# Optimization experiments

Measured on AMD Instinct MI355X. Metric: run time of the kernel, lower is better.

The kernel has to match this reference:

```python
import jax, jax.numpy as jnp
import numpy as np

DIM = 128
HEADS = 4
LOGIT_MAX = float(np.log(1.0 / 0.01))  # log(100)


def setup_inputs() -> dict:
    root = jax.random.key(0)
    ks = jax.random.split(root, 10)
    B, nH, nW, Lq, Lv, C = 16, 16, 16, 64, 64, DIM
    s = 0.02
    return {
        "query": jax.random.normal(ks[0], (B, nH, nW, Lq, C), jnp.float32),
        "key": jax.random.normal(ks[1], (B, nH, nW, Lv, C), jnp.float32),
        "value": jax.random.normal(ks[2], (B, nH, nW, Lv, C), jnp.float32),
        "position": jax.random.normal(ks[3], (B, HEADS, Lq, Lv), jnp.float32),
        # torch nn.Linear convention: weight [out_features, in_features]
        "Wq": jax.random.normal(ks[4], (C, C), jnp.float32) * s,
        "bq": jnp.zeros((C,), jnp.float32),
        "Wk": jax.random.normal(ks[5], (C, C), jnp.float32) * s,  # fc_key has no bias
        "Wv": jax.random.normal(ks[6], (C, C), jnp.float32) * s,
        "bv": jnp.zeros((C,), jnp.float32),
        "Wp": jax.random.normal(ks[7], (C, C), jnp.float32) * s,
        "bp": jnp.zeros((C,), jnp.float32),
        "logit_scale": jnp.log(10.0) * jnp.ones((HEADS, 1, 1), jnp.float32),
    }


def reference(query, key, value, position, Wq, bq, Wk, Wv, bv, Wp, bp, logit_scale):
    B, nH, nW, Lq, C = query.shape
    Lv = key.shape[3]
    H = logit_scale.shape[0]
    d = C // H
    # QKV projections, split heads: [B,nH,nW,H,L,d]
    q = (query @ Wq.T + bq).reshape(B, nH, nW, Lq, H, d).swapaxes(3, 4)
    k = (key @ Wk.T).reshape(B, nH, nW, Lv, H, d).swapaxes(3, 4)
    v = (value @ Wv.T + bv).reshape(B, nH, nW, Lv, H, d).swapaxes(3, 4)
    # clamped learned per-head logit scale
    scale = jnp.exp(jnp.minimum(logit_scale, LOGIT_MAX))  # [H,1,1]
    attn = jnp.einsum('bijhqd,bijhkd->bijhqk', q, k) * scale
    attn = attn + position[:, None, None]  # broadcast over window grid (nH,nW)
    attn = jax.nn.softmax(attn, axis=-1)
    x = jnp.einsum('bijhqk,bijhkd->bijhqd', attn, v)
    x = x.swapaxes(3, 4).reshape(B, nH, nW, Lq, C)
    x = x @ Wp.T + bp
    return (x, attn)
```

## Files before the change

### kernel.cpp

```cpp
#include <hip/hip_runtime.h>

using f16   = _Float16;
using f16x4 = __attribute__((ext_vector_type(4))) _Float16;
using f16x8 = __attribute__((ext_vector_type(8))) _Float16;
using f32x4 = __attribute__((ext_vector_type(4))) float;

#define DEVI __device__ __forceinline__

namespace {
constexpr int S_XQ  = 0;
constexpr int S_XK  = 16384;
constexpr int S_SCR = 32768;
constexpr float LOGIT_MAX_C = 4.6051701859880914f;
constexpr float L2E = 1.4426950408889634f;
}

DEVI int swzA(int row, int b) { return (row << 8) + (b ^ ((row & 7) << 4)); }
DEVI int swz64(int row, int b) { return (row << 6) + (b ^ (((row >> 1) & 3) << 4)); }

DEVI f16x8 ldA(const char* base, int row, int k0) {
  return *reinterpret_cast<const f16x8*>(base + swzA(row, k0 << 1));
}

DEVI void stage_in(const float* __restrict__ src, char* __restrict__ dst, int tid) {
#pragma unroll
  for (int i = 0; i < 8; ++i) {
    int f = tid + (i << 8);
    float4 v = reinterpret_cast<const float4*>(src)[f];
    f16x4 h;
    h[0] = (f16)v.x; h[1] = (f16)v.y; h[2] = (f16)v.z; h[3] = (f16)v.w;
    *reinterpret_cast<f16x4*>(dst + swzA(f >> 5, (f & 31) << 3)) = h;
  }
}

DEVI void proj_acc(const char* __restrict__ xb, const f16* __restrict__ Wm,
                   f32x4 (&acc)[4][2], int w, int lr, int lg) {
#pragma unroll
  for (int mt = 0; mt < 4; ++mt)
#pragma unroll
    for (int n = 0; n < 2; ++n)
      acc[mt][n] = f32x4{0.f, 0.f, 0.f, 0.f};
#pragma unroll
  for (int kt = 0; kt < 4; ++kt) {
    f16x8 b0 = *reinterpret_cast<const f16x8*>(Wm + (w * 32 + lr) * 128 + kt * 32 + lg * 8);
    f16x8 b1 = *reinterpret_cast<const f16x8*>(Wm + (w * 32 + 16 + lr) * 128 + kt * 32 + lg * 8);
#pragma unroll
    for (int mt = 0; mt < 4; ++mt) {
      f16x8 a = ldA(xb, mt * 16 + lr, kt * 32 + lg * 8);
      acc[mt][0] = __builtin_amdgcn_mfma_f32_16x16x32_f16(a, b0, acc[mt][0], 0, 0, 0);
      acc[mt][1] = __builtin_amdgcn_mfma_f32_16x16x32_f16(a, b1, acc[mt][1], 0, 0, 0);
    }
  }
}

DEVI void epi_scr64(const f32x4 (&acc)[4][2], char* __restrict__ scr,
                    const float* __restrict__ bias, int lr, int lg) {
  float b0 = bias ? bias[lr] : 0.f;
  float b1 = bias ? bias[16 + lr] : 0.f;
#pragma unroll
  for (int mt = 0; mt < 4; ++mt)
#pragma unroll
    for (int n = 0; n < 2; ++n)
#pragma unroll
      for (int r = 0; r < 4; ++r) {
        int row = mt * 16 + lg * 4 + r;
        *reinterpret_cast<f16*>(scr + swz64(row, (n * 16 + lr) << 1)) =
            (f16)(acc[mt][n][r] + (n ? b1 : b0));
      }
}
DEVI f16x8 ldS64(const char* __restrict__ scr, int row, int lg) {
  return *reinterpret_cast<const f16x8*>(scr + swz64(row, lg << 4));
}

DEVI void epi_rowmajor(const f32x4 (&acc)[4][2], char* __restrict__ dst,
                       int w, int lr, int lg) {
#pragma unroll
  for (int mt = 0; mt < 4; ++mt)
#pragma unroll
    for (int n = 0; n < 2; ++n)
#pragma unroll
      for (int r = 0; r < 4; ++r) {
        int row = mt * 16 + lg * 4 + r;
        int col = w * 32 + n * 16 + lr;
        *reinterpret_cast<f16*>(dst + swzA(row, col << 1)) = (f16)acc[mt][n][r];
      }
}

__global__ void wcvt_kernel(const float* __restrict__ Wq, const float* __restrict__ Wk,
                            const float* __restrict__ Wv, const float* __restrict__ Wp,
                            f16* __restrict__ W16) {
  int idx = blockIdx.x * 256 + threadIdx.x;
  int m = idx >> 12;
  int off = (idx & 4095) << 2;
  const float* src = m == 0 ? Wq : m == 1 ? Wk : m == 2 ? Wv : Wp;
  float4 v = *reinterpret_cast<const float4*>(src + off);
  f16x4 h;
  h[0] = (f16)v.x; h[1] = (f16)v.y; h[2] = (f16)v.z; h[3] = (f16)v.w;
  *reinterpret_cast<f16x4*>(W16 + (m << 14) + off) = h;
}

__global__ __launch_bounds__(256, 3)
void fpca_kernel(const float* __restrict__ q_in, const float* __restrict__ k_in,
                 const float* __restrict__ v_in, const float* __restrict__ pos_in,
                 const f16* __restrict__ W16,
                 const float* __restrict__ bq, const float* __restrict__ bv,
                 const float* __restrict__ bp, const float* __restrict__ lsc,
                 float* __restrict__ d_x, float* __restrict__ d_attn) {
  __shared__ char smem[49152];
  const int tid = threadIdx.x;
  const int w = tid >> 6;
  const int lane = tid & 63;
  const int lr = lane & 15;
  const int lg = lane >> 4;
  const int win = blockIdx.x;
  const int b = win >> 8;
  const size_t winOff = (size_t)win << 13;
  const f16* Wq16 = W16;
  const f16* Wk16 = W16 + 16384;
  const f16* Wv16 = W16 + 32768;
  const f16* Wp16 = W16 + 49152;
  char* scr = smem + S_SCR + (w << 12);

  stage_in(q_in + winOff, smem + S_XQ, tid);
  stage_in(k_in + winOff, smem + S_XK, tid);
  const float4* vsrc = reinterpret_cast<const float4*>(v_in + winOff);
  f16x4 pfh[8];
#pragma unroll
  for (int i = 0; i < 8; ++i) {
    float4 v = vsrc[tid + (i << 8)];
    pfh[i][0] = (f16)v.x; pfh[i][1] = (f16)v.y;
    pfh[i][2] = (f16)v.z; pfh[i][3] = (f16)v.w;
  }
  __syncthreads();

  f32x4 acc[4][2];
  proj_acc(smem + S_XQ, Wq16, acc, w, lr, lg);
  epi_scr64(acc, scr, bq + w * 32, lr, lg);
  f16x8 bQ[4];
#pragma unroll
  for (int nt = 0; nt < 4; ++nt) bQ[nt] = ldS64(scr, nt * 16 + lr, lg);

  proj_acc(smem + S_XK, Wk16, acc, w, lr, lg);
  epi_scr64(acc, scr, nullptr, lr, lg);
  f16x8 aK[4];
#pragma unroll
  for (int mt = 0; mt < 4; ++mt) aK[mt] = ldS64(scr, mt * 16 + lr, lg);
  __syncthreads();

#pragma unroll
  for (int i = 0; i < 8; ++i) {
    int f = tid + (i << 8);
    *reinterpret_cast<f16x4*>(smem + S_XK + swzA(f >> 5, (f & 31) << 3)) = pfh[i];
  }

  const float scale = exp2f(fminf(lsc[w], LOGIT_MAX_C) * L2E);
  const float* pos = pos_in + (((size_t)b * 4 + w) << 12);
  float* attn_out = d_attn + (((size_t)win * 4 + w) << 12);
  f16x4 P16[4][4];
#pragma unroll
  for (int nt = 0; nt < 4; ++nt) {
    f32x4 s[4];
#pragma unroll
    for (int mt = 0; mt < 4; ++mt) s[mt] = f32x4{0.f, 0.f, 0.f, 0.f};
#pragma unroll
    for (int mt = 0; mt < 4; ++mt)
      s[mt] = __builtin_amdgcn_mfma_f32_16x16x32_f16(aK[mt], bQ[nt], s[mt], 0, 0, 0);
    const int q = nt * 16 + lr;
#pragma unroll
    for (int mt = 0; mt < 4; ++mt) {
      float4 pv = *reinterpret_cast<const float4*>(pos + (q << 6) + mt * 16 + lg * 4);
      s[mt][0] = s[mt][0] * scale + pv.x;
      s[mt][1] = s[mt][1] * scale + pv.y;
      s[mt][2] = s[mt][2] * scale + pv.z;
      s[mt][3] = s[mt][3] * scale + pv.w;
    }
    float m = s[0][0];
#pragma unroll
    for (int mt = 0; mt < 4; ++mt)
#pragma unroll
      for (int r = 0; r < 4; ++r) m = fmaxf(m, s[mt][r]);
    m = fmaxf(m, __shfl_xor(m, 16));
    m = fmaxf(m, __shfl_xor(m, 32));
    float sum = 0.f;
#pragma unroll
    for (int mt = 0; mt < 4; ++mt)
#pragma unroll
      for (int r = 0; r < 4; ++r) {
        float e = exp2f((s[mt][r] - m) * L2E);
        s[mt][r] = e;
        sum += e;
      }
    sum += __shfl_xor(sum, 16);
    sum += __shfl_xor(sum, 32);
    float rinv = __builtin_amdgcn_rcpf(sum);
#pragma unroll
    for (int mt = 0; mt < 4; ++mt) {
      float4 o;
      o.x = (s[mt][0] *= rinv);
      o.y = (s[mt][1] *= rinv);
      o.z = (s[mt][2] *= rinv);
      o.w = (s[mt][3] *= rinv);
      *reinterpret_cast<float4*>(attn_out + (q << 6) + mt * 16 + lg * 4) = o;
      P16[mt][nt][0] = (f16)s[mt][0];
      P16[mt][nt][1] = (f16)s[mt][1];
      P16[mt][nt][2] = (f16)s[mt][2];
      P16[mt][nt][3] = (f16)s[mt][3];
    }
  }

#define WR_P(MT)                                                                   \
  {                                                                                \
    _Pragma("unroll") for (int nt = 0; nt < 4; ++nt) {                             \
      const int q = nt * 16 + lr;                                                  \
      *reinterpret_cast<f16x4*>(scr + (q << 6) +                                   \
          (((((MT) & 1) << 5) + (lg << 3)) ^ (((q >> 1) & 3) << 4))) =             \
          P16[MT][nt];                                                             \
    }                                                                              \
  }
  f16x8 aP[4][2];
#pragma unroll
  for (int h = 0; h < 2; ++h) {
    WR_P(2 * h)
    WR_P(2 * h + 1)
#pragma unroll
    for (int mt = 0; mt < 4; ++mt) {
      const int q = mt * 16 + lr;
      aP[mt][h] = *reinterpret_cast<const f16x8*>(scr + (q << 6) +
          ((lg << 4) ^ (((q >> 1) & 3) << 4)));
    }
  }
  __syncthreads();

  proj_acc(smem + S_XK, Wv16, acc, w, lr, lg);
  {
    float c0 = bv[w * 32 + lr], c1 = bv[w * 32 + 16 + lr];
#pragma unroll
    for (int mt = 0; mt < 4; ++mt)
#pragma unroll
      for (int n = 0; n < 2; ++n) {
        int d = n * 16 + lr;
        f16x4 h;
        h[0] = (f16)(acc[mt][n][0] + (n ? c1 : c0));
        h[1] = (f16)(acc[mt][n][1] + (n ? c1 : c0));
        h[2] = (f16)(acc[mt][n][2] + (n ? c1 : c0));
        h[3] = (f16)(acc[mt][n][3] + (n ? c1 : c0));
        *reinterpret_cast<f16x4*>(scr + (d << 7) +
            ((mt * 32 + lg * 8) ^ ((d & 7) << 4))) = h;
      }
  }
  f16x8 bV[2][2];
#pragma unroll
  for (int n = 0; n < 2; ++n)
#pragma unroll
    for (int kt = 0; kt < 2; ++kt) {
      int d = n * 16 + lr;
      bV[n][kt] = *reinterpret_cast<const f16x8*>(scr + (d << 7) +
          ((kt * 64 + lg * 16) ^ ((d & 7) << 4)));
    }

  f32x4 oacc[4][2];
#pragma unroll
  for (int mt = 0; mt < 4; ++mt)
#pragma unroll
    for (int n = 0; n < 2; ++n)
      oacc[mt][n] = f32x4{0.f, 0.f, 0.f, 0.f};
#pragma unroll
  for (int mt = 0; mt < 4; ++mt)
#pragma unroll
    for (int kt = 0; kt < 2; ++kt) {
      oacc[mt][0] = __builtin_amdgcn_mfma_f32_16x16x32_f16(aP[mt][kt], bV[0][kt], oacc[mt][0], 0, 0, 0);
      oacc[mt][1] = __builtin_amdgcn_mfma_f32_16x16x32_f16(aP[mt][kt], bV[1][kt], oacc[mt][1], 0, 0, 0);
    }

  epi_rowmajor(oacc, smem + S_XQ, w, lr, lg);
  __syncthreads();

  f32x4 xacc[4][2];
  proj_acc(smem + S_XQ, Wp16, xacc, w, lr, lg);
  const float b0 = bp[w * 32 + lr];
  const float b1 = bp[w * 32 + 16 + lr];
  float* xo = d_x + winOff;
#pragma unroll
  for (int mt = 0; mt < 4; ++mt)
#pragma unroll
    for (int n = 0; n < 2; ++n)
#pragma unroll
      for (int r = 0; r < 4; ++r) {
        int row = mt * 16 + lg * 4 + r;
        int col = w * 32 + n * 16 + lr;
        xo[(row << 7) + col] = xacc[mt][n][r] + (n ? b1 : b0);
      }
}

extern "C" void kernel_launch(void* const* d_in, const int* in_sizes, int n_in,
                              void* d_out, int out_size, void* d_ws, size_t ws_size,
                              hipStream_t stream) {
  const float* q   = (const float*)d_in[0];
  const float* k   = (const float*)d_in[1];
  const float* v   = (const float*)d_in[2];
  const float* pos = (const float*)d_in[3];
  const float* Wq  = (const float*)d_in[4];
  const float* bq  = (const float*)d_in[5];
  const float* Wk  = (const float*)d_in[6];
  const float* Wv  = (const float*)d_in[7];
  const float* bv  = (const float*)d_in[8];
  const float* Wp  = (const float*)d_in[9];
  const float* bp  = (const float*)d_in[10];
  const float* ls  = (const float*)d_in[11];
  f16* W16 = (f16*)d_ws;
  float* d_x    = (float*)d_out;
  float* d_attn = d_x + (size_t)16 * 16 * 16 * 64 * 128;
  wcvt_kernel<<<64, 256, 0, stream>>>(Wq, Wk, Wv, Wp, W16);
  fpca_kernel<<<4096, 256, 0, stream>>>(q, k, v, pos, W16, bq, bv, bp, ls,
                                        d_x, d_attn);
}
```

Baseline: 205.6 us.

## Load value operand directly from global and drop two block barriers

The value projection now reads fp32 value rows straight from global memory into MFMA A-operands, converting them on the fly. This replaces the register prefetch, the LDS staging and the barrier that guarded it. The attention output is written to each wave's own scratch slice, and the output projection reads across those four slices, which removes the row-major epilogue and the barrier before the V projection. Fewer barriers and no LDS round trip for V, at the cost of uncoalesced 32-byte global reads per lane that are repeated across the four waves, and the loss of the early V prefetch overlap.

New measurement: 273.4 us. +33.0%, slower.

```diff
diff --git a/kernel.cpp b/kernel.cpp
--- a/kernel.cpp
+++ b/kernel.cpp
@@ -33,6 +33,15 @@
   }
 }
 
+DEVI f16x8 ld_g8(const float* __restrict__ G, int row, int k0) {
+  const float4* p = reinterpret_cast<const float4*>(G + row * 128 + k0);
+  float4 a = p[0], c = p[1];
+  f16x8 r;
+  r[0] = (f16)a.x; r[1] = (f16)a.y; r[2] = (f16)a.z; r[3] = (f16)a.w;
+  r[4] = (f16)c.x; r[5] = (f16)c.y; r[6] = (f16)c.z; r[7] = (f16)c.w;
+  return r;
+}
+
 DEVI void proj_acc(const char* __restrict__ xb, const f16* __restrict__ Wm,
                    f32x4 (&acc)[4][2], int w, int lr, int lg) {
 #pragma unroll
@@ -70,20 +79,6 @@
 }
 DEVI f16x8 ldS64(const char* __restrict__ scr, int row, int lg) {
   return *reinterpret_cast<const f16x8*>(scr + swz64(row, lg << 4));
-}
-
-DEVI void epi_rowmajor(const f32x4 (&acc)[4][2], char* __restrict__ dst,
-                       int w, int lr, int lg) {
-#pragma unroll
-  for (int mt = 0; mt < 4; ++mt)
-#pragma unroll
-    for (int n = 0; n < 2; ++n)
-#pragma unroll
-      for (int r = 0; r < 4; ++r) {
-        int row = mt * 16 + lg * 4 + r;
-        int col = w * 32 + n * 16 + lr;
-        *reinterpret_cast<f16*>(dst + swzA(row, col << 1)) = (f16)acc[mt][n][r];
-      }
 }
 
 __global__ void wcvt_kernel(const float* __restrict__ Wq, const float* __restrict__ Wk,
@@ -123,14 +118,6 @@
 
   stage_in(q_in + winOff, smem + S_XQ, tid);
   stage_in(k_in + winOff, smem + S_XK, tid);
-  const float4* vsrc = reinterpret_cast<const float4*>(v_in + winOff);
-  f16x4 pfh[8];
-#pragma unroll
-  for (int i = 0; i < 8; ++i) {
-    float4 v = vsrc[tid + (i << 8)];
-    pfh[i][0] = (f16)v.x; pfh[i][1] = (f16)v.y;
-    pfh[i][2] = (f16)v.z; pfh[i][3] = (f16)v.w;
-  }
   __syncthreads();
 
   f32x4 acc[4][2];
@@ -145,13 +132,6 @@
   f16x8 aK[4];
 #pragma unroll
   for (int mt = 0; mt < 4; ++mt) aK[mt] = ldS64(scr, mt * 16 + lr, lg);
-  __syncthreads();
-
-#pragma unroll
-  for (int i = 0; i < 8; ++i) {
-    int f = tid + (i << 8);
-    *reinterpret_cast<f16x4*>(smem + S_XK + swzA(f >> 5, (f & 31) << 3)) = pfh[i];
-  }
 
   const float scale = exp2f(fminf(lsc[w], LOGIT_MAX_C) * L2E);
   const float* pos = pos_in + (((size_t)b * 4 + w) << 12);
@@ -229,9 +209,27 @@
           ((lg << 4) ^ (((q >> 1) & 3) << 4)));
     }
   }
-  __syncthreads();
-
-  proj_acc(smem + S_XK, Wv16, acc, w, lr, lg);
+#undef WR_P
+
+  {
+    const float* Xv = v_in + winOff;
+#pragma unroll
+    for (int mt = 0; mt < 4; ++mt)
+#pragma unroll
+      for (int n = 0; n < 2; ++n)
+        acc[mt][n] = f32x4{0.f, 0.f, 0.f, 0.f};
+#pragma unroll
+    for (int kt = 0; kt < 4; ++kt) {
+      f16x8 b0 = *reinterpret_cast<const f16x8*>(Wv16 + (w * 32 + lr) * 128 + kt * 32 + lg * 8);
+      f16x8 b1 = *reinterpret_cast<const f16x8*>(Wv16 + (w * 32 + 16 + lr) * 128 + kt * 32 + lg * 8);
+#pragma unroll
+      for (int mt = 0; mt < 4; ++mt) {
+        f16x8 a = ld_g8(Xv, mt * 16 + lr, kt * 32 + lg * 8);
+        acc[mt][0] = __builtin_amdgcn_mfma_f32_16x16x32_f16(a, b0, acc[mt][0], 0, 0, 0);
+        acc[mt][1] = __builtin_amdgcn_mfma_f32_16x16x32_f16(a, b1, acc[mt][1], 0, 0, 0);
+      }
+    }
+  }
   {
     float c0 = bv[w * 32 + lr], c1 = bv[w * 32 + 16 + lr];
 #pragma unroll
@@ -272,11 +270,27 @@
       oacc[mt][1] = __builtin_amdgcn_mfma_f32_16x16x32_f16(aP[mt][kt], bV[1][kt], oacc[mt][1], 0, 0, 0);
     }
 
-  epi_rowmajor(oacc, smem + S_XQ, w, lr, lg);
+  epi_scr64(oacc, scr, nullptr, lr, lg);
   __syncthreads();
 
   f32x4 xacc[4][2];
-  proj_acc(smem + S_XQ, Wp16, xacc, w, lr, lg);
+#pragma unroll
+  for (int mt = 0; mt < 4; ++mt)
+#pragma unroll
+    for (int n = 0; n < 2; ++n)
+      xacc[mt][n] = f32x4{0.f, 0.f, 0.f, 0.f};
+#pragma unroll
+  for (int kt = 0; kt < 4; ++kt) {
+    const char* oscr = smem + S_SCR + (kt << 12);
+    f16x8 b0 = *reinterpret_cast<const f16x8*>(Wp16 + (w * 32 + lr) * 128 + kt * 32 + lg * 8);
+    f16x8 b1 = *reinterpret_cast<const f16x8*>(Wp16 + (w * 32 + 16 + lr) * 128 + kt * 32 + lg * 8);
+#pragma unroll
+    for (int mt = 0; mt < 4; ++mt) {
+      f16x8 a = ldS64(oscr, mt * 16 + lr, lg);
+      xacc[mt][0] = __builtin_amdgcn_mfma_f32_16x16x32_f16(a, b0, xacc[mt][0], 0, 0, 0);
+      xacc[mt][1] = __builtin_amdgcn_mfma_f32_16x16x32_f16(a, b1, xacc[mt][1], 0, 0, 0);
+    }
+  }
   const float b0 = bp[w * 32 + lr];
   const float b1 = bp[w * 32 + 16 + lr];
   float* xo = d_x + winOff;
```

## Replace LDS scratch transposes with cross-lane shuffles for Q/K/V/P fragments

Applied to the files above, without the earlier changes.

Q and K projections are now computed transposed (weights as the A operand), so the accumulator layout can be rearranged into MFMA operand fragments with lane shuffles instead of a round trip through per-wave LDS scratch. The V and P fragment handoffs also move from LDS stores and loads to shuffle-based gathers. This removes the 16 KB scratch region, cutting shared memory per block from 48 KB to 32 KB, which could allow more resident blocks. The cost is many ds_bpermute-style shuffles and selects per fragment, and possibly higher register pressure.

Result: slower. 238.0 us (+15.8%).

```diff
diff --git a/kernel.cpp b/kernel.cpp
--- a/kernel.cpp
+++ b/kernel.cpp
@@ -8,15 +8,13 @@
 #define DEVI __device__ __forceinline__
 
 namespace {
-constexpr int S_XQ  = 0;
-constexpr int S_XK  = 16384;
-constexpr int S_SCR = 32768;
+constexpr int S_XQ = 0;
+constexpr int S_XK = 16384;
 constexpr float LOGIT_MAX_C = 4.6051701859880914f;
 constexpr float L2E = 1.4426950408889634f;
 }
 
 DEVI int swzA(int row, int b) { return (row << 8) + (b ^ ((row & 7) << 4)); }
-DEVI int swz64(int row, int b) { return (row << 6) + (b ^ (((row >> 1) & 3) << 4)); }
 
 DEVI f16x8 ldA(const char* base, int row, int k0) {
   return *reinterpret_cast<const f16x8*>(base + swzA(row, k0 << 1));
@@ -33,6 +31,55 @@
   }
 }
 
+DEVI f16x4 shfl4(f16x4 v, int src) {
+  int2 t = __builtin_bit_cast(int2, v);
+  int2 r;
+  r.x = __shfl(t.x, src);
+  r.y = __shfl(t.y, src);
+  return __builtin_bit_cast(f16x4, r);
+}
+DEVI f16x8 gather_frag(f16x4 p0, f16x4 p1, int s0, int s1, int lg) {
+  f16x4 a0 = shfl4(p0, s0), a1 = shfl4(p0, s1);
+  f16x4 b0 = shfl4(p1, s0), b1 = shfl4(p1, s1);
+  f16x4 lo = (lg & 2) ? b0 : a0;
+  f16x4 hi = (lg & 2) ? b1 : a1;
+  f16x8 r;
+  r[0] = lo[0]; r[1] = lo[1]; r[2] = lo[2]; r[3] = lo[3];
+  r[4] = hi[0]; r[5] = hi[1]; r[6] = hi[2]; r[7] = hi[3];
+  return r;
+}
+DEVI f16x4 pack4(f32x4 a) {
+  f16x4 h;
+  h[0] = (f16)a[0]; h[1] = (f16)a[1]; h[2] = (f16)a[2]; h[3] = (f16)a[3];
+  return h;
+}
+DEVI f16x4 pack4b(f32x4 a, float4 b) {
+  f16x4 h;
+  h[0] = (f16)(a[0] + b.x); h[1] = (f16)(a[1] + b.y);
+  h[2] = (f16)(a[2] + b.z); h[3] = (f16)(a[3] + b.w);
+  return h;
+}
+
+DEVI void projT_acc(const char* __restrict__ xb, const f16* __restrict__ Wm,
+                    f32x4 (&acc)[2][4], int w, int lr, int lg) {
+#pragma unroll
+  for (int ft = 0; ft < 2; ++ft)
+#pragma unroll
+    for (int t = 0; t < 4; ++t)
+      acc[ft][t] = f32x4{0.f, 0.f, 0.f, 0.f};
+#pragma unroll
+  for (int kt = 0; kt < 4; ++kt) {
+    f16x8 w0 = *reinterpret_cast<const f16x8*>(Wm + (w * 32 + lr) * 128 + kt * 32 + lg * 8);
+    f16x8 w1 = *reinterpret_cast<const f16x8*>(Wm + (w * 32 + 16 + lr) * 128 + kt * 32 + lg * 8);
+#pragma unroll
+    for (int t = 0; t < 4; ++t) {
+      f16x8 x = ldA(xb, t * 16 + lr, kt * 32 + lg * 8);
+      acc[0][t] = __builtin_amdgcn_mfma_f32_16x16x32_f16(w0, x, acc[0][t], 0, 0, 0);
+      acc[1][t] = __builtin_amdgcn_mfma_f32_16x16x32_f16(w1, x, acc[1][t], 0, 0, 0);
+    }
+  }
+}
+
 DEVI void proj_acc(const char* __restrict__ xb, const f16* __restrict__ Wm,
                    f32x4 (&acc)[4][2], int w, int lr, int lg) {
 #pragma unroll
@@ -51,25 +98,6 @@
       acc[mt][1] = __builtin_amdgcn_mfma_f32_16x16x32_f16(a, b1, acc[mt][1], 0, 0, 0);
     }
   }
-}
-
-DEVI void epi_scr64(const f32x4 (&acc)[4][2], char* __restrict__ scr,
-                    const float* __restrict__ bias, int lr, int lg) {
-  float b0 = bias ? bias[lr] : 0.f;
-  float b1 = bias ? bias[16 + lr] : 0.f;
-#pragma unroll
-  for (int mt = 0; mt < 4; ++mt)
-#pragma unroll
-    for (int n = 0; n < 2; ++n)
-#pragma unroll
-      for (int r = 0; r < 4; ++r) {
-        int row = mt * 16 + lg * 4 + r;
-        *reinterpret_cast<f16*>(scr + swz64(row, (n * 16 + lr) << 1)) =
-            (f16)(acc[mt][n][r] + (n ? b1 : b0));
-      }
-}
-DEVI f16x8 ldS64(const char* __restrict__ scr, int row, int lg) {
-  return *reinterpret_cast<const f16x8*>(scr + swz64(row, lg << 4));
 }
 
 DEVI void epi_rowmajor(const f32x4 (&acc)[4][2], char* __restrict__ dst,
@@ -106,12 +134,14 @@
                  const float* __restrict__ bq, const float* __restrict__ bv,
                  const float* __restrict__ bp, const float* __restrict__ lsc,
                  float* __restrict__ d_x, float* __restrict__ d_attn) {
-  __shared__ char smem[49152];
+  __shared__ char smem[32768];
   const int tid = threadIdx.x;
   const int w = tid >> 6;
   const int lane = tid & 63;
   const int lr = lane & 15;
   const int lg = lane >> 4;
+  const int s0 = lr + ((lane & 16) << 1);
+  const int s1 = s0 + 16;
   const int win = blockIdx.x;
   const int b = win >> 8;
   const size_t winOff = (size_t)win << 13;
@@ -119,7 +149,6 @@
   const f16* Wk16 = W16 + 16384;
   const f16* Wv16 = W16 + 32768;
   const f16* Wp16 = W16 + 49152;
-  char* scr = smem + S_SCR + (w << 12);
 
   stage_in(q_in + winOff, smem + S_XQ, tid);
   stage_in(k_in + winOff, smem + S_XK, tid);
@@ -133,18 +162,20 @@
   }
   __syncthreads();
 
-  f32x4 acc[4][2];
-  proj_acc(smem + S_XQ, Wq16, acc, w, lr, lg);
-  epi_scr64(acc, scr, bq + w * 32, lr, lg);
+  f32x4 accT[2][4];
+  projT_acc(smem + S_XQ, Wq16, accT, w, lr, lg);
+  float4 bq0 = *reinterpret_cast<const float4*>(bq + w * 32 + lg * 4);
+  float4 bq1 = *reinterpret_cast<const float4*>(bq + w * 32 + 16 + lg * 4);
   f16x8 bQ[4];
 #pragma unroll
-  for (int nt = 0; nt < 4; ++nt) bQ[nt] = ldS64(scr, nt * 16 + lr, lg);
-
-  proj_acc(smem + S_XK, Wk16, acc, w, lr, lg);
-  epi_scr64(acc, scr, nullptr, lr, lg);
+  for (int nt = 0; nt < 4; ++nt)
+    bQ[nt] = gather_frag(pack4b(accT[0][nt], bq0), pack4b(accT[1][nt], bq1), s0, s1, lg);
+
+  projT_acc(smem + S_XK, Wk16, accT, w, lr, lg);
   f16x8 aK[4];
 #pragma unroll
-  for (int mt = 0; mt < 4; ++mt) aK[mt] = ldS64(scr, mt * 16 + lr, lg);
+  for (int mt = 0; mt < 4; ++mt)
+    aK[mt] = gather_frag(pack4(accT[0][mt]), pack4(accT[1][mt]), s0, s1, lg);
   __syncthreads();
 
 #pragma unroll
@@ -207,56 +238,27 @@
       P16[mt][nt][3] = (f16)s[mt][3];
     }
   }
-
-#define WR_P(MT)                                                                   \
-  {                                                                                \
-    _Pragma("unroll") for (int nt = 0; nt < 4; ++nt) {                             \
-      const int q = nt * 16 + lr;                                                  \
-      *reinterpret_cast<f16x4*>(scr + (q << 6) +                                   \
-          (((((MT) & 1) << 5) + (lg << 3)) ^ (((q >> 1) & 3) << 4))) =             \
-          P16[MT][nt];                                                             \
-    }                                                                              \
-  }
-  f16x8 aP[4][2];
-#pragma unroll
-  for (int h = 0; h < 2; ++h) {
-    WR_P(2 * h)
-    WR_P(2 * h + 1)
-#pragma unroll
-    for (int mt = 0; mt < 4; ++mt) {
-      const int q = mt * 16 + lr;
-      aP[mt][h] = *reinterpret_cast<const f16x8*>(scr + (q << 6) +
-          ((lg << 4) ^ (((q >> 1) & 3) << 4)));
-    }
-  }
   __syncthreads();
 
-  proj_acc(smem + S_XK, Wv16, acc, w, lr, lg);
+  f32x4 vacc[4][2];
+  proj_acc(smem + S_XK, Wv16, vacc, w, lr, lg);
+  f16x8 bV[2][2];
   {
     float c0 = bv[w * 32 + lr], c1 = bv[w * 32 + 16 + lr];
 #pragma unroll
-    for (int mt = 0; mt < 4; ++mt)
-#pragma unroll
-      for (int n = 0; n < 2; ++n) {
-        int d = n * 16 + lr;
-        f16x4 h;
-        h[0] = (f16)(acc[mt][n][0] + (n ? c1 : c0));
-        h[1] = (f16)(acc[mt][n][1] + (n ? c1 : c0));
-        h[2] = (f16)(acc[mt][n][2] + (n ? c1 : c0));
-        h[3] = (f16)(acc[mt][n][3] + (n ? c1 : c0));
-        *reinterpret_cast<f16x4*>(scr + (d << 7) +
-            ((mt * 32 + lg * 8) ^ ((d & 7) << 4))) = h;
+    for (int n = 0; n < 2; ++n) {
+      float c = n ? c1 : c0;
+      f16x4 pV[4];
+#pragma unroll
+      for (int mt = 0; mt < 4; ++mt) {
+        f32x4 t = vacc[mt][n];
+        t[0] += c; t[1] += c; t[2] += c; t[3] += c;
+        pV[mt] = pack4(t);
       }
-  }
-  f16x8 bV[2][2];
-#pragma unroll
-  for (int n = 0; n < 2; ++n)
-#pragma unroll
-    for (int kt = 0; kt < 2; ++kt) {
-      int d = n * 16 + lr;
-      bV[n][kt] = *reinterpret_cast<const f16x8*>(scr + (d << 7) +
-          ((kt * 64 + lg * 16) ^ ((d & 7) << 4)));
-    }
+      bV[n][0] = gather_frag(pV[0], pV[1], s0, s1, lg);
+      bV[n][1] = gather_frag(pV[2], pV[3], s0, s1, lg);
+    }
+  }
 
   f32x4 oacc[4][2];
 #pragma unroll
@@ -265,11 +267,12 @@
     for (int n = 0; n < 2; ++n)
       oacc[mt][n] = f32x4{0.f, 0.f, 0.f, 0.f};
 #pragma unroll
-  for (int mt = 0; mt < 4; ++mt)
-#pragma unroll
-    for (int kt = 0; kt < 2; ++kt) {
-      oacc[mt][0] = __builtin_amdgcn_mfma_f32_16x16x32_f16(aP[mt][kt], bV[0][kt], oacc[mt][0], 0, 0, 0);
-      oacc[mt][1] = __builtin_amdgcn_mfma_f32_16x16x32_f16(aP[mt][kt], bV[1][kt], oacc[mt][1], 0, 0, 0);
+  for (int kt = 0; kt < 2; ++kt)
+#pragma unroll
+    for (int mt = 0; mt < 4; ++mt) {
+      f16x8 aPx = gather_frag(P16[2 * kt][mt], P16[2 * kt + 1][mt], s0, s1, lg);
+      oacc[mt][0] = __builtin_amdgcn_mfma_f32_16x16x32_f16(aPx, bV[0][kt], oacc[mt][0], 0, 0, 0);
+      oacc[mt][1] = __builtin_amdgcn_mfma_f32_16x16x32_f16(aPx, bV[1][kt], oacc[mt][1], 0, 0, 0);
     }
 
   epi_rowmajor(oacc, smem + S_XQ, w, lr, lg);
```

## Split each window across 8 warps by halving query rows per warp

Applied to the files above, without the earlier changes.

The block grows from 256 to 512 threads, so each head is handled by two warps that each own half of the 64 query/token rows. Projections, softmax, PV and the output projection are all split by row half. Shared-memory scratch is reorganised into per-head Q/K regions plus per-warp P scratch, and extra barriers are added so K and V can be shared across the two halves. The aim is more waves per window and lower per-thread register pressure to hide latency. The cost is more LDS (64KB per block), extra synchronisation, and duplicated weight-fragment loads per warp.

Result: slower. 253.3 us (+23.2%).

```diff
diff --git a/kernel.cpp b/kernel.cpp
--- a/kernel.cpp
+++ b/kernel.cpp
@@ -24,8 +24,8 @@
 
 DEVI void stage_in(const float* __restrict__ src, char* __restrict__ dst, int tid) {
 #pragma unroll
-  for (int i = 0; i < 8; ++i) {
-    int f = tid + (i << 8);
+  for (int i = 0; i < 4; ++i) {
+    int f = tid + (i << 9);
     float4 v = reinterpret_cast<const float4*>(src)[f];
     f16x4 h;
     h[0] = (f16)v.x; h[1] = (f16)v.y; h[2] = (f16)v.z; h[3] = (f16)v.w;
@@ -33,57 +33,43 @@
   }
 }
 
-DEVI void proj_acc(const char* __restrict__ xb, const f16* __restrict__ Wm,
-                   f32x4 (&acc)[4][2], int w, int lr, int lg) {
-#pragma unroll
-  for (int mt = 0; mt < 4; ++mt)
-#pragma unroll
-    for (int n = 0; n < 2; ++n)
-      acc[mt][n] = f32x4{0.f, 0.f, 0.f, 0.f};
+DEVI void proj_split(const char* __restrict__ xb, const f16* __restrict__ Wm,
+                     f32x4 (&acc)[2][2], int w, int hf, int lr, int lg) {
+#pragma unroll
+  for (int mtl = 0; mtl < 2; ++mtl)
+#pragma unroll
+    for (int n = 0; n < 2; ++n)
+      acc[mtl][n] = f32x4{0.f, 0.f, 0.f, 0.f};
 #pragma unroll
   for (int kt = 0; kt < 4; ++kt) {
     f16x8 b0 = *reinterpret_cast<const f16x8*>(Wm + (w * 32 + lr) * 128 + kt * 32 + lg * 8);
     f16x8 b1 = *reinterpret_cast<const f16x8*>(Wm + (w * 32 + 16 + lr) * 128 + kt * 32 + lg * 8);
 #pragma unroll
-    for (int mt = 0; mt < 4; ++mt) {
-      f16x8 a = ldA(xb, mt * 16 + lr, kt * 32 + lg * 8);
-      acc[mt][0] = __builtin_amdgcn_mfma_f32_16x16x32_f16(a, b0, acc[mt][0], 0, 0, 0);
-      acc[mt][1] = __builtin_amdgcn_mfma_f32_16x16x32_f16(a, b1, acc[mt][1], 0, 0, 0);
-    }
-  }
-}
-
-DEVI void epi_scr64(const f32x4 (&acc)[4][2], char* __restrict__ scr,
-                    const float* __restrict__ bias, int lr, int lg) {
+    for (int mtl = 0; mtl < 2; ++mtl) {
+      f16x8 a = ldA(xb, hf * 32 + mtl * 16 + lr, kt * 32 + lg * 8);
+      acc[mtl][0] = __builtin_amdgcn_mfma_f32_16x16x32_f16(a, b0, acc[mtl][0], 0, 0, 0);
+      acc[mtl][1] = __builtin_amdgcn_mfma_f32_16x16x32_f16(a, b1, acc[mtl][1], 0, 0, 0);
+    }
+  }
+}
+
+DEVI void epi_half(const f32x4 (&acc)[2][2], char* __restrict__ scr,
+                   const float* __restrict__ bias, int hf, int lr, int lg) {
   float b0 = bias ? bias[lr] : 0.f;
   float b1 = bias ? bias[16 + lr] : 0.f;
 #pragma unroll
-  for (int mt = 0; mt < 4; ++mt)
+  for (int mtl = 0; mtl < 2; ++mtl)
 #pragma unroll
     for (int n = 0; n < 2; ++n)
 #pragma unroll
       for (int r = 0; r < 4; ++r) {
-        int row = mt * 16 + lg * 4 + r;
+        int row = hf * 32 + mtl * 16 + lg * 4 + r;
         *reinterpret_cast<f16*>(scr + swz64(row, (n * 16 + lr) << 1)) =
-            (f16)(acc[mt][n][r] + (n ? b1 : b0));
+            (f16)(acc[mtl][n][r] + (n ? b1 : b0));
       }
 }
 DEVI f16x8 ldS64(const char* __restrict__ scr, int row, int lg) {
   return *reinterpret_cast<const f16x8*>(scr + swz64(row, lg << 4));
-}
-
-DEVI void epi_rowmajor(const f32x4 (&acc)[4][2], char* __restrict__ dst,
-                       int w, int lr, int lg) {
-#pragma unroll
-  for (int mt = 0; mt < 4; ++mt)
-#pragma unroll
-    for (int n = 0; n < 2; ++n)
-#pragma unroll
-      for (int r = 0; r < 4; ++r) {
-        int row = mt * 16 + lg * 4 + r;
-        int col = w * 32 + n * 16 + lr;
-        *reinterpret_cast<f16*>(dst + swzA(row, col << 1)) = (f16)acc[mt][n][r];
-      }
 }
 
 __global__ void wcvt_kernel(const float* __restrict__ Wq, const float* __restrict__ Wk,
@@ -99,16 +85,18 @@
   *reinterpret_cast<f16x4*>(W16 + (m << 14) + off) = h;
 }
 
-__global__ __launch_bounds__(256, 3)
+__global__ __launch_bounds__(512, 4)
 void fpca_kernel(const float* __restrict__ q_in, const float* __restrict__ k_in,
                  const float* __restrict__ v_in, const float* __restrict__ pos_in,
                  const f16* __restrict__ W16,
                  const float* __restrict__ bq, const float* __restrict__ bv,
                  const float* __restrict__ bp, const float* __restrict__ lsc,
                  float* __restrict__ d_x, float* __restrict__ d_attn) {
-  __shared__ char smem[49152];
+  __shared__ char smem[65536];
   const int tid = threadIdx.x;
-  const int w = tid >> 6;
+  const int W = tid >> 6;
+  const int w = W & 3;
+  const int hf = W >> 2;
   const int lane = tid & 63;
   const int lr = lane & 15;
   const int lg = lane >> 4;
@@ -119,53 +107,56 @@
   const f16* Wk16 = W16 + 16384;
   const f16* Wv16 = W16 + 32768;
   const f16* Wp16 = W16 + 49152;
-  char* scr = smem + S_SCR + (w << 12);
+  char* Qscr = smem + S_SCR + (w << 13);
+  char* Kscr = Qscr + 4096;
+  char* Pscr = smem + S_XQ + (W << 11);
 
   stage_in(q_in + winOff, smem + S_XQ, tid);
   stage_in(k_in + winOff, smem + S_XK, tid);
   const float4* vsrc = reinterpret_cast<const float4*>(v_in + winOff);
-  f16x4 pfh[8];
-#pragma unroll
-  for (int i = 0; i < 8; ++i) {
-    float4 v = vsrc[tid + (i << 8)];
+  f16x4 pfh[4];
+#pragma unroll
+  for (int i = 0; i < 4; ++i) {
+    float4 v = vsrc[tid + (i << 9)];
     pfh[i][0] = (f16)v.x; pfh[i][1] = (f16)v.y;
     pfh[i][2] = (f16)v.z; pfh[i][3] = (f16)v.w;
   }
   __syncthreads();
 
-  f32x4 acc[4][2];
-  proj_acc(smem + S_XQ, Wq16, acc, w, lr, lg);
-  epi_scr64(acc, scr, bq + w * 32, lr, lg);
-  f16x8 bQ[4];
-#pragma unroll
-  for (int nt = 0; nt < 4; ++nt) bQ[nt] = ldS64(scr, nt * 16 + lr, lg);
-
-  proj_acc(smem + S_XK, Wk16, acc, w, lr, lg);
-  epi_scr64(acc, scr, nullptr, lr, lg);
+  f32x4 acc[2][2];
+  proj_split(smem + S_XQ, Wq16, acc, w, hf, lr, lg);
+  epi_half(acc, Qscr, bq + w * 32, hf, lr, lg);
+  f16x8 bQ[2];
+#pragma unroll
+  for (int ntl = 0; ntl < 2; ++ntl)
+    bQ[ntl] = ldS64(Qscr, hf * 32 + ntl * 16 + lr, lg);
+
+  proj_split(smem + S_XK, Wk16, acc, w, hf, lr, lg);
+  epi_half(acc, Kscr, nullptr, hf, lr, lg);
+  __syncthreads();
+
+#pragma unroll
+  for (int i = 0; i < 4; ++i) {
+    int f = tid + (i << 9);
+    *reinterpret_cast<f16x4*>(smem + S_XK + swzA(f >> 5, (f & 31) << 3)) = pfh[i];
+  }
   f16x8 aK[4];
 #pragma unroll
-  for (int mt = 0; mt < 4; ++mt) aK[mt] = ldS64(scr, mt * 16 + lr, lg);
-  __syncthreads();
-
-#pragma unroll
-  for (int i = 0; i < 8; ++i) {
-    int f = tid + (i << 8);
-    *reinterpret_cast<f16x4*>(smem + S_XK + swzA(f >> 5, (f & 31) << 3)) = pfh[i];
-  }
+  for (int mt = 0; mt < 4; ++mt) aK[mt] = ldS64(Kscr, mt * 16 + lr, lg);
 
   const float scale = exp2f(fminf(lsc[w], LOGIT_MAX_C) * L2E);
   const float* pos = pos_in + (((size_t)b * 4 + w) << 12);
   float* attn_out = d_attn + (((size_t)win * 4 + w) << 12);
-  f16x4 P16[4][4];
-#pragma unroll
-  for (int nt = 0; nt < 4; ++nt) {
+  f16x4 P16[4][2];
+#pragma unroll
+  for (int ntl = 0; ntl < 2; ++ntl) {
     f32x4 s[4];
 #pragma unroll
     for (int mt = 0; mt < 4; ++mt) s[mt] = f32x4{0.f, 0.f, 0.f, 0.f};
 #pragma unroll
     for (int mt = 0; mt < 4; ++mt)
-      s[mt] = __builtin_amdgcn_mfma_f32_16x16x32_f16(aK[mt], bQ[nt], s[mt], 0, 0, 0);
-    const int q = nt * 16 + lr;
+      s[mt] = __builtin_amdgcn_mfma_f32_16x16x32_f16(aK[mt], bQ[ntl], s[mt], 0, 0, 0);
+    const int q = hf * 32 + ntl * 16 + lr;
 #pragma unroll
     for (int mt = 0; mt < 4; ++mt) {
       float4 pv = *reinterpret_cast<const float4*>(pos + (q << 6) + mt * 16 + lg * 4);
@@ -201,94 +192,105 @@
       o.z = (s[mt][2] *= rinv);
       o.w = (s[mt][3] *= rinv);
       *reinterpret_cast<float4*>(attn_out + (q << 6) + mt * 16 + lg * 4) = o;
-      P16[mt][nt][0] = (f16)s[mt][0];
-      P16[mt][nt][1] = (f16)s[mt][1];
-      P16[mt][nt][2] = (f16)s[mt][2];
-      P16[mt][nt][3] = (f16)s[mt][3];
+      P16[mt][ntl][0] = (f16)s[mt][0];
+      P16[mt][ntl][1] = (f16)s[mt][1];
+      P16[mt][ntl][2] = (f16)s[mt][2];
+      P16[mt][ntl][3] = (f16)s[mt][3];
     }
   }
 
 #define WR_P(MT)                                                                   \
   {                                                                                \
-    _Pragma("unroll") for (int nt = 0; nt < 4; ++nt) {                             \
-      const int q = nt * 16 + lr;                                                  \
-      *reinterpret_cast<f16x4*>(scr + (q << 6) +                                   \
-          (((((MT) & 1) << 5) + (lg << 3)) ^ (((q >> 1) & 3) << 4))) =             \
-          P16[MT][nt];                                                             \
+    _Pragma("unroll") for (int ntl = 0; ntl < 2; ++ntl) {                          \
+      const int row = ntl * 16 + lr;                                               \
+      *reinterpret_cast<f16x4*>(Pscr + (row << 6) +                                \
+          (((((MT) & 1) << 5) + (lg << 3)) ^ (((row >> 1) & 3) << 4))) =           \
+          P16[MT][ntl];                                                            \
     }                                                                              \
   }
-  f16x8 aP[4][2];
+  f16x8 aP[2][2];
 #pragma unroll
   for (int h = 0; h < 2; ++h) {
     WR_P(2 * h)
     WR_P(2 * h + 1)
 #pragma unroll
-    for (int mt = 0; mt < 4; ++mt) {
-      const int q = mt * 16 + lr;
-      aP[mt][h] = *reinterpret_cast<const f16x8*>(scr + (q << 6) +
-          ((lg << 4) ^ (((q >> 1) & 3) << 4)));
-    }
-  }
-  __syncthreads();
-
-  proj_acc(smem + S_XK, Wv16, acc, w, lr, lg);
+    for (int qt = 0; qt < 2; ++qt) {
+      const int row = qt * 16 + lr;
+      aP[qt][h] = *reinterpret_cast<const f16x8*>(Pscr + (row << 6) +
+          ((lg << 4) ^ (((row >> 1) & 3) << 4)));
+    }
+  }
+#undef WR_P
+  __syncthreads();
+
+  proj_split(smem + S_XK, Wv16, acc, w, hf, lr, lg);
   {
     float c0 = bv[w * 32 + lr], c1 = bv[w * 32 + 16 + lr];
 #pragma unroll
-    for (int mt = 0; mt < 4; ++mt)
+    for (int mtl = 0; mtl < 2; ++mtl)
 #pragma unroll
       for (int n = 0; n < 2; ++n) {
         int d = n * 16 + lr;
         f16x4 h;
-        h[0] = (f16)(acc[mt][n][0] + (n ? c1 : c0));
-        h[1] = (f16)(acc[mt][n][1] + (n ? c1 : c0));
-        h[2] = (f16)(acc[mt][n][2] + (n ? c1 : c0));
-        h[3] = (f16)(acc[mt][n][3] + (n ? c1 : c0));
-        *reinterpret_cast<f16x4*>(scr + (d << 7) +
-            ((mt * 32 + lg * 8) ^ ((d & 7) << 4))) = h;
-      }
-  }
+        h[0] = (f16)(acc[mtl][n][0] + (n ? c1 : c0));
+        h[1] = (f16)(acc[mtl][n][1] + (n ? c1 : c0));
+        h[2] = (f16)(acc[mtl][n][2] + (n ? c1 : c0));
+        h[3] = (f16)(acc[mtl][n][3] + (n ? c1 : c0));
+        *reinterpret_cast<f16x4*>(Kscr + (d << 7) +
+            ((hf * 64 + mtl * 32 + lg * 8) ^ ((d & 7) << 4))) = h;
+      }
+  }
+  __syncthreads();
+
   f16x8 bV[2][2];
 #pragma unroll
   for (int n = 0; n < 2; ++n)
 #pragma unroll
     for (int kt = 0; kt < 2; ++kt) {
       int d = n * 16 + lr;
-      bV[n][kt] = *reinterpret_cast<const f16x8*>(scr + (d << 7) +
+      bV[n][kt] = *reinterpret_cast<const f16x8*>(Kscr + (d << 7) +
           ((kt * 64 + lg * 16) ^ ((d & 7) << 4)));
     }
-
-  f32x4 oacc[4][2];
-#pragma unroll
-  for (int mt = 0; mt < 4; ++mt)
-#pragma unroll
-    for (int n = 0; n < 2; ++n)
-      oacc[mt][n] = f32x4{0.f, 0.f, 0.f, 0.f};
-#pragma unroll
-  for (int mt = 0; mt < 4; ++mt)
+  f32x4 oacc[2][2];
+#pragma unroll
+  for (int qt = 0; qt < 2; ++qt)
+#pragma unroll
+    for (int n = 0; n < 2; ++n)
+      oacc[qt][n] = f32x4{0.f, 0.f, 0.f, 0.f};
+#pragma unroll
+  for (int qt = 0; qt < 2; ++qt)
 #pragma unroll
     for (int kt = 0; kt < 2; ++kt) {
-      oacc[mt][0] = __builtin_amdgcn_mfma_f32_16x16x32_f16(aP[mt][kt], bV[0][kt], oacc[mt][0], 0, 0, 0);
-      oacc[mt][1] = __builtin_amdgcn_mfma_f32_16x16x32_f16(aP[mt][kt], bV[1][kt], oacc[mt][1], 0, 0, 0);
-    }
-
-  epi_rowmajor(oacc, smem + S_XQ, w, lr, lg);
-  __syncthreads();
-
-  f32x4 xacc[4][2];
-  proj_acc(smem + S_XQ, Wp16, xacc, w, lr, lg);
+      oacc[qt][0] = __builtin_amdgcn_mfma_f32_16x16x32_f16(aP[qt][kt], bV[0][kt], oacc[qt][0], 0, 0, 0);
+      oacc[qt][1] = __builtin_amdgcn_mfma_f32_16x16x32_f16(aP[qt][kt], bV[1][kt], oacc[qt][1], 0, 0, 0);
+    }
+
+#pragma unroll
+  for (int qt = 0; qt < 2; ++qt)
+#pragma unroll
+    for (int n = 0; n < 2; ++n)
+#pragma unroll
+      for (int r = 0; r < 4; ++r) {
+        int row = hf * 32 + qt * 16 + lg * 4 + r;
+        int col = w * 32 + n * 16 + lr;
+        *reinterpret_cast<f16*>(smem + S_XQ + swzA(row, col << 1)) = (f16)oacc[qt][n][r];
+      }
+  __syncthreads();
+
+  f32x4 xacc[2][2];
+  proj_split(smem + S_XQ, Wp16, xacc, w, hf, lr, lg);
   const float b0 = bp[w * 32 + lr];
   const float b1 = bp[w * 32 + 16 + lr];
   float* xo = d_x + winOff;
 #pragma unroll
-  for (int mt = 0; mt < 4; ++mt)
+  for (int mtl = 0; mtl < 2; ++mtl)
 #pragma unroll
     for (int n = 0; n < 2; ++n)
 #pragma unroll
       for (int r = 0; r < 4; ++r) {
-        int row = mt * 16 + lg * 4 + r;
+        int row = hf * 32 + mtl * 16 + lg * 4 + r;
         int col = w * 32 + n * 16 + lr;
-        xo[(row << 7) + col] = xacc[mt][n][r] + (n ? b1 : b0);
+        xo[(row << 7) + col] = xacc[mtl][n][r] + (n ? b1 : b0);
       }
 }
 
@@ -311,6 +313,6 @@
   float* d_x    = (float*)d_out;
   float* d_attn = d_x + (size_t)16 * 16 * 16 * 64 * 128;
   wcvt_kernel<<<64, 256, 0, stream>>>(Wq, Wk, Wv, Wp, W16);
-  fpca_kernel<<<4096, 256, 0, stream>>>(q, k, v, pos, W16, bq, bv, bp, ls,
+  fpca_kernel<<<4096, 512, 0, stream>>>(q, k, v, pos, W16, bq, bv, bp, ls,
                                         d_x, d_attn);
 }
```
